# Kernel tuning notes

Measured on AMD Instinct MI355X. Metric: run time of the kernel, lower is better.

Reference implementation:

```python
import jax, jax.numpy as jnp
import numpy as np

DIM = 1024
NUM_HEADS = 16
HEAD_DIM = DIM // NUM_HEADS
SCALE = DIM ** (-0.5)  # NOTE: original scales by full dim, not head_dim


def setup_inputs() -> dict:
    key = jax.random.key(0)
    ks = jax.random.split(key, 5)
    B, S = 2, 2048
    x = jax.random.normal(ks[0], (B, S, DIM), dtype=jnp.float32)
    w_qkv = jax.random.normal(ks[1], (DIM, 3 * DIM), dtype=jnp.float32) * (DIM ** -0.5)
    b_qkv = jax.random.normal(ks[2], (3 * DIM,), dtype=jnp.float32) * 0.02
    w_proj = jax.random.normal(ks[3], (DIM, DIM), dtype=jnp.float32) * (DIM ** -0.5)
    b_proj = jax.random.normal(ks[4], (DIM,), dtype=jnp.float32) * 0.02
    return {"x": x, "w_qkv": w_qkv, "b_qkv": b_qkv, "w_proj": w_proj, "b_proj": b_proj}


def reference(x, w_qkv, b_qkv, w_proj, b_proj):
    B, S, D = x.shape
    qkv = x @ w_qkv + b_qkv                                  # [B,S,3D]
    qkv = qkv.reshape(B, S, NUM_HEADS, 3 * HEAD_DIM).transpose(0, 2, 1, 3)  # [B,H,S,3hd]
    q, k, v = jnp.split(qkv, 3, axis=-1)                     # each [B,H,S,hd]
    attn = jnp.einsum("bhqd,bhkd->bhqk", q, k) * SCALE       # [B,H,S,S]
    attn = jax.nn.softmax(attn, axis=-1)
    out = jnp.einsum("bhqk,bhkd->bhqd", attn, v)             # [B,H,S,hd]
    out = out.transpose(0, 2, 1, 3).reshape(B, S, D)
    return out @ w_proj + b_proj
```

## Files before the change

kernel.cpp:

```cpp
#include <hip/hip_runtime.h>
#include <hip/hip_bf16.h>

#define DIM 1024
#define NH 16
#define HD 64
#define BB 2
#define SS 2048
#define MROWS (BB * SS)
#define SCALE 0.03125f
#define SC_LOG2E 0.04508422002778011f

typedef unsigned short u16;
typedef unsigned int u32;
typedef __attribute__((ext_vector_type(8))) short short8;
typedef __attribute__((ext_vector_type(4))) float f32x4;
typedef __attribute__((ext_vector_type(2))) unsigned int u32x2;

#if __has_builtin(__builtin_amdgcn_exp2f)
#define EXP2(x) __builtin_amdgcn_exp2f(x)
#else
#define EXP2(x) __builtin_exp2f(x)
#endif

__device__ __forceinline__ u16 f2bf(float f) {
  union { float f; u32 u; } v; v.f = f;
  return (u16)((v.u + 0x7fffu + ((v.u >> 16) & 1u)) >> 16);
}

__device__ __forceinline__ u32 pack2bf(float a, float b) {
  union { __hip_bfloat162 h; u32 u; } cv;
  cv.h = __float22bfloat162_rn(make_float2(a, b));
  return cv.u;
}

__device__ __forceinline__ void plswap32(u32& a, u32& b) {
#if __has_builtin(__builtin_amdgcn_permlane32_swap)
  u32x2 t = __builtin_amdgcn_permlane32_swap(a, b, false, false);
  a = t[0]; b = t[1];
#else
  asm("v_permlane32_swap_b32 %0, %1" : "+v"(a), "+v"(b));
#endif
}
__device__ __forceinline__ void plswap16(u32& a, u32& b) {
#if __has_builtin(__builtin_amdgcn_permlane16_swap)
  u32x2 t = __builtin_amdgcn_permlane16_swap(a, b, false, false);
  a = t[0]; b = t[1];
#else
  asm("v_permlane16_swap_b32 %0, %1" : "+v"(a), "+v"(b));
#endif
}

__device__ __forceinline__ void async16(const u16* g, u16* l) {
  __builtin_amdgcn_global_load_lds(
      (const __attribute__((address_space(1))) void*)(const void*)g,
      (__attribute__((address_space(3))) void*)(void*)l, 16, 0, 0);
}

__device__ __forceinline__ short8 ld8(const u16* p) { return *(const short8*)p; }

__global__ void cvt_kernel(const float* __restrict__ in, u16* __restrict__ out, int n4) {
  int i = blockIdx.x * blockDim.x + threadIdx.x;
  if (i < n4) {
    float4 v = ((const float4*)in)[i];
    u32 lo = (u32)f2bf(v.x) | ((u32)f2bf(v.y) << 16);
    u32 hi = (u32)f2bf(v.z) | ((u32)f2bf(v.w) << 16);
    ((uint2*)out)[i] = make_uint2(lo, hi);
  }
}

__global__ void tconv_kernel(const float* __restrict__ in, u16* __restrict__ out, int R, int C) {
  __shared__ u16 t[64 * 65];
  int c0 = blockIdx.x * 64, r0 = blockIdx.y * 64;
  #pragma unroll
  for (int i = 0; i < 16; i++) {
    int j = i * 256 + threadIdx.x;
    int rr = j >> 6, cc = j & 63;
    t[rr * 65 + cc] = f2bf(in[(size_t)(r0 + rr) * C + c0 + cc]);
  }
  __syncthreads();
  #pragma unroll
  for (int i = 0; i < 16; i++) {
    int j = i * 256 + threadIdx.x;
    int oc = j >> 6, orr = j & 63;
    out[(size_t)(c0 + oc) * R + r0 + orr] = t[orr * 65 + oc];
  }
}

template <int MODE>
__global__ __launch_bounds__(256, 2) void gemm_bt(
    const u16* __restrict__ A, const u16* __restrict__ Bt,
    const float* __restrict__ bias, void* __restrict__ C,
    u16* __restrict__ vT, int M, int N, int K) {
  __shared__ __align__(16) u16 As[128 * 32];
  __shared__ __align__(16) u16 Bs[128 * 32];
  const int tid = threadIdx.x;
  const int w = tid >> 6, l = tid & 63;
  const int r = l & 15, q = l >> 4;
  const int m0 = blockIdx.y * 128, n0 = blockIdx.x * 128;
  const int qm = (w & 1) * 64, qn = (w >> 1) * 64;

  const size_t aoff = (size_t)(m0 + w * 16 + (l >> 2)) * K + (size_t)(l & 3) * 8;
  const size_t boff = (size_t)(n0 + w * 16 + (l >> 2)) * K + (size_t)(l & 3) * 8;
  u16* alds = &As[(w * 64 + l) * 8];
  u16* blds = &Bs[(w * 64 + l) * 8];

  f32x4 acc[4][4] = {};
  for (int k0 = 0; k0 < K; k0 += 32) {
    async16(A + aoff + k0, alds);
    async16(A + aoff + (size_t)64 * K + k0, alds + 2048);
    async16(Bt + boff + k0, blds);
    async16(Bt + boff + (size_t)64 * K + k0, blds + 2048);
    __syncthreads();
    short8 af[4], bfr[4];
    #pragma unroll
    for (int i = 0; i < 4; i++) af[i] = ld8(&As[(qm + i * 16 + r) * 32 + q * 8]);
    #pragma unroll
    for (int j = 0; j < 4; j++) bfr[j] = ld8(&Bs[(qn + j * 16 + r) * 32 + q * 8]);
    #pragma unroll
    for (int i = 0; i < 4; i++)
      #pragma unroll
      for (int j = 0; j < 4; j++)
        acc[i][j] = __builtin_amdgcn_mfma_f32_16x16x32_bf16(af[i], bfr[j], acc[i][j], 0, 0, 0);
    __syncthreads();
  }
  #pragma unroll
  for (int i = 0; i < 4; i++) {
    int ro = m0 + qm + i * 16 + q * 4;
    #pragma unroll
    for (int j = 0; j < 4; j++) {
      int col = n0 + qn + j * 16 + r;
      float bv = bias[col];
      float v0 = acc[i][j][0] + bv, v1 = acc[i][j][1] + bv;
      float v2 = acc[i][j][2] + bv, v3 = acc[i][j][3] + bv;
      if (MODE == 1) {
        float* out = (float*)C;
        out[(size_t)(ro + 0) * N + col] = v0;
        out[(size_t)(ro + 1) * N + col] = v1;
        out[(size_t)(ro + 2) * N + col] = v2;
        out[(size_t)(ro + 3) * N + col] = v3;
      } else {
        int h = col / 192, wi = col - h * 192;
        if (wi >= 128) {
          int bb = ro >> 11, s = ro & 2047, d = wi - 128;
          uint2 pk = make_uint2(pack2bf(v0, v1), pack2bf(v2, v3));
          *(uint2*)&vT[((size_t)((bb * NH + h) * HD + d)) * SS + s] = pk;
        } else {
          u16* qk2 = (u16*)C;
          const float sc = (wi < 64) ? SC_LOG2E : 1.0f;
          qk2[(size_t)(ro + 0) * 2048 + h * 128 + wi] = f2bf(v0 * sc);
          qk2[(size_t)(ro + 1) * 2048 + h * 128 + wi] = f2bf(v1 * sc);
          qk2[(size_t)(ro + 2) * 2048 + h * 128 + wi] = f2bf(v2 * sc);
          qk2[(size_t)(ro + 3) * 2048 + h * 128 + wi] = f2bf(v3 * sc);
        }
      }
    }
  }
}

__global__ __launch_bounds__(512, 4) void attn6_kernel(
    const u16* __restrict__ qk2, const u16* __restrict__ vT,
    u16* __restrict__ attno) {
  __shared__ __align__(16) u16 smem[32768];
  const int tid = threadIdx.x;
  const int w = tid >> 6, l = tid & 63;
  const int r = l & 15, q = l >> 4;
  const int wq = w & 3, ws = w >> 2;
  const int lin = blockIdx.x + 16 * (blockIdx.y + 16 * blockIdx.z);
  const int k8 = lin & 7, jj = lin >> 3;
  const int bh = ((jj >> 4) << 3) + k8;
  const int h = bh & 15, b = bh >> 4;
  const int q0 = (jj & 15) * 128;

  const u16* qb = qk2 + (size_t)b * SS * 2048;
  const u16* kB = qb + h * 128 + 64;
  const u16* vB = vT + (size_t)((b * NH + h) * HD) * SS;

  short8 qf[2][2];
  #pragma unroll
  for (int i = 0; i < 2; i++)
    #pragma unroll
    for (int kq = 0; kq < 2; kq++)
      qf[i][kq] = ld8(qb + (size_t)(q0 + wq * 32 + i * 16 + r) * 2048 + h * 128 + kq * 32 + q * 8);

  const int klrow = l >> 3;
  const int kchunk = (l & 7) ^ klrow;
  const int vlrow = l >> 4;
  const int vslot = l & 15;

#define STAGE(KV0, DST) do {                                                     \
    u16* Kd_ = (DST); u16* Vd_ = Kd_ + 8192;                                     \
    _Pragma("unroll")                                                            \
    for (int tt = 0; tt < 2; tt++) {                                             \
      int g = w * 2 + tt;                                                        \
      async16(kB + (size_t)((KV0) + g * 8 + klrow) * 2048 + kchunk * 8,          \
              &Kd_[g * 512 + l * 8]);                                            \
    }                                                                            \
    _Pragma("unroll")                                                            \
    for (int tt = 0; tt < 2; tt++) {                                             \
      int g = w * 2 + tt;                                                        \
      int d_ = g * 4 + vlrow;                                                    \
      int c_ = vslot ^ (d_ & 15);                                                \
      async16(vB + (size_t)d_ * SS + (KV0) + c_ * 8, &Vd_[g * 512 + l * 8]);     \
    }                                                                            \
  } while (0)

#define CONV(ks) do {                                                            \
    _Pragma("unroll")                                                            \
    for (int i = 0; i < 2; i++) {                                                \
      f32x4 sa = sacc[(ks) * 2][i], sb = sacc[(ks) * 2 + 1][i];                  \
      u32 A0 = pack2bf(EXP2(sa[0]), EXP2(sa[1]));                                \
      u32 A1 = pack2bf(EXP2(sa[2]), EXP2(sa[3]));                                \
      u32 B0 = pack2bf(EXP2(sb[0]), EXP2(sb[1]));                                \
      u32 B1 = pack2bf(EXP2(sb[2]), EXP2(sb[3]));                                \
      plswap32(A0, B0);                                                          \
      plswap32(A1, B1);                                                          \
      plswap16(A0, B0);                                                          \
      plswap16(A1, B1);                                                          \
      union { short8 s8; u32 u[4]; } pk;                                         \
      pk.u[0] = A0; pk.u[1] = A1; pk.u[2] = B0; pk.u[3] = B1;                    \
      pa[ks][i] = pk.s8;                                                         \
    }                                                                            \
  } while (0)

#define QKT(j2) do {                                                             \
    const u16* krow = &Ks[(ws * 64 + (j2) * 16 + r) * 64];                       \
    short8 a0 = ld8(krow + ((q ^ (r & 7)) * 8));                                 \
    short8 a1 = ld8(krow + (((4 + q) ^ (r & 7)) * 8));                           \
    __builtin_amdgcn_s_setprio(1);                                               \
    _Pragma("unroll")                                                            \
    for (int i = 0; i < 2; i++) {                                                \
      sacc[j2][i] = __builtin_amdgcn_mfma_f32_16x16x32_bf16(a0, qf[i][0], sacc[j2][i], 0, 0, 0); \
      sacc[j2][i] = __builtin_amdgcn_mfma_f32_16x16x32_bf16(a1, qf[i][1], sacc[j2][i], 0, 0, 0); \
    }                                                                            \
    __builtin_amdgcn_s_setprio(0);                                               \
  } while (0)

#define PV(ks) do {                                                              \
    __builtin_amdgcn_s_setprio(1);                                               \
    den[0] = __builtin_amdgcn_mfma_f32_16x16x32_bf16(pa[ks][0], vone, den[0], 0, 0, 0); \
    den[1] = __builtin_amdgcn_mfma_f32_16x16x32_bf16(pa[ks][1], vone, den[1], 0, 0, 0); \
    _Pragma("unroll")                                                            \
    for (int dj = 0; dj < 4; dj++) {                                             \
      short8 vb = ld8(&Vs[(dj * 16 + r) * 128 + (((ws * 8 + (ks) * 4 + q) ^ r) * 8)]); \
      oacc[0][dj] = __builtin_amdgcn_mfma_f32_16x16x32_bf16(pa[ks][0], vb, oacc[0][dj], 0, 0, 0); \
      oacc[1][dj] = __builtin_amdgcn_mfma_f32_16x16x32_bf16(pa[ks][1], vb, oacc[1][dj], 0, 0, 0); \
    }                                                                            \
    __builtin_amdgcn_s_setprio(0);                                               \
  } while (0)

  const short8 vone = {0x3F80, 0x3F80, 0x3F80, 0x3F80, 0x3F80, 0x3F80, 0x3F80, 0x3F80};
  f32x4 oacc[2][4] = {};
  f32x4 den[2] = {};

  STAGE(0, smem);
  __syncthreads();

  for (int t = 0; t < 16; ++t) {
    const int cur = t & 1;
    u16* Ks = smem + cur * 16384;
    u16* Vs = Ks + 8192;
    if (t < 15) STAGE((t + 1) * 128, smem + (cur ^ 1) * 16384);

    f32x4 sacc[4][2] = {};
    short8 pa[2][2];
    QKT(0); QKT(1);
    CONV(0);
    QKT(2); QKT(3);
    PV(0);
    CONV(1);
    PV(1);
    __syncthreads();
  }
#undef STAGE
#undef CONV
#undef QKT
#undef PV

  float* part = (float*)smem;
  float* dnf  = part + 8 * 32 * 36;
  const int ho = 1 - ws;
  {
    const int wbase = (wq * 2 + ho) * 32;
    #pragma unroll
    for (int i = 0; i < 2; i++) {
      if (ws == 0) {
        *(f32x4*)&part[(wbase + r) * 36 + i * 16 + q * 4]      = oacc[i][2];
        *(f32x4*)&part[(wbase + 16 + r) * 36 + i * 16 + q * 4] = oacc[i][3];
      } else {
        *(f32x4*)&part[(wbase + r) * 36 + i * 16 + q * 4]      = oacc[i][0];
        *(f32x4*)&part[(wbase + 16 + r) * 36 + i * 16 + q * 4] = oacc[i][1];
      }
      if (r == 0)
        *(f32x4*)&dnf[(ws * 4 + wq) * 32 + i * 16 + q * 4] = den[i];
    }
  }
  __syncthreads();
  {
    const int rbase = (wq * 2 + ws) * 32;
    #pragma unroll
    for (int i = 0; i < 2; i++) {
      f32x4 dt = *(f32x4*)&dnf[(ho * 4 + wq) * 32 + i * 16 + q * 4] + den[i];
      f32x4 oa, ob;
      if (ws == 0) { oa = oacc[i][0]; ob = oacc[i][1]; }
      else         { oa = oacc[i][2]; ob = oacc[i][3]; }
      oa += *(f32x4*)&part[(rbase + r) * 36 + i * 16 + q * 4];
      ob += *(f32x4*)&part[(rbase + 16 + r) * 36 + i * 16 + q * 4];
      #pragma unroll
      for (int e = 0; e < 4; e++) {
        float di = 1.f / dt[e];
        int row = q0 + wq * 32 + i * 16 + q * 4 + e;
        u16* o = &attno[(size_t)(b * SS + row) * DIM + h * HD + ws * 32 + r];
        o[0]  = f2bf(oa[e] * di);
        o[16] = f2bf(ob[e] * di);
      }
    }
  }
}

extern "C" void kernel_launch(void* const* d_in, const int* in_sizes, int n_in,
                              void* d_out, int out_size, void* d_ws, size_t ws_size,
                              hipStream_t stream) {
  const float* x      = (const float*)d_in[0];
  const float* w_qkv  = (const float*)d_in[1];
  const float* b_qkv  = (const float*)d_in[2];
  const float* w_proj = (const float*)d_in[3];
  const float* b_proj = (const float*)d_in[4];
  float* out = (float*)d_out;
  char* ws = (char*)d_ws;
  u16* xb     = (u16*)(ws);
  u16* wqkvT  = (u16*)(ws + ((size_t)8  << 20));
  u16* wprojT = (u16*)(ws + ((size_t)14 << 20));
  u16* qk2    = (u16*)(ws + ((size_t)16 << 20));
  u16* attno  = (u16*)(ws + ((size_t)32 << 20));
  u16* vT     = (u16*)(ws + ((size_t)40 << 20));

  cvt_kernel<<<4096, 256, 0, stream>>>(x, xb, MROWS * DIM / 4);
  tconv_kernel<<<dim3(48, 16), 256, 0, stream>>>(w_qkv, wqkvT, DIM, 3 * DIM);
  tconv_kernel<<<dim3(16, 16), 256, 0, stream>>>(w_proj, wprojT, DIM, DIM);
  gemm_bt<0><<<dim3(24, 32), 256, 0, stream>>>(xb, wqkvT, b_qkv, qk2, vT, MROWS, 3 * DIM, DIM);
  attn6_kernel<<<dim3(16, NH, BB), 512, 0, stream>>>(qk2, vT, attno);
  gemm_bt<1><<<dim3(8, 32), 256, 0, stream>>>(attno, wprojT, b_proj, out, nullptr, MROWS, DIM, DIM);
}
```

Before: 189.1 us.

## Double-buffer GEMM LDS stages, add XCD-aware block swizzle and 128x64 projection tiles

The GEMM kernels now double-buffer their shared-memory tiles, so the async global-to-LDS load for the next K step is issued before the MFMAs on the current step. This removes one barrier per iteration. Blocks are launched on a 1D grid and remapped so that consecutive blocks landing on the same XCD (lin & 7) cover adjacent tiles, which should improve L2 reuse. The output projection gets a new 128x64-tile kernel with 512 blocks instead of 256, to fill the 256 CUs better. The cost is double the LDS per block, which can lower occupancy.

```diff
diff --git a/kernel.cpp b/kernel.cpp
--- a/kernel.cpp
+++ b/kernel.cpp
@@ -86,31 +86,41 @@
   }
 }
 
-template <int MODE>
+template <int MODE, int NXB>
 __global__ __launch_bounds__(256, 2) void gemm_bt(
     const u16* __restrict__ A, const u16* __restrict__ Bt,
     const float* __restrict__ bias, void* __restrict__ C,
     u16* __restrict__ vT, int M, int N, int K) {
-  __shared__ __align__(16) u16 As[128 * 32];
-  __shared__ __align__(16) u16 Bs[128 * 32];
+  __shared__ __align__(16) u16 smem[16384];
   const int tid = threadIdx.x;
   const int w = tid >> 6, l = tid & 63;
   const int r = l & 15, q = l >> 4;
-  const int m0 = blockIdx.y * 128, n0 = blockIdx.x * 128;
+  const int nwg = gridDim.x;
+  const int cpx = nwg >> 3;
+  const int lin = blockIdx.x;
+  const int swz = (lin & 7) * cpx + (lin >> 3);
+  const int m0 = (swz / NXB) * 128, n0 = (swz % NXB) * 128;
   const int qm = (w & 1) * 64, qn = (w >> 1) * 64;
 
   const size_t aoff = (size_t)(m0 + w * 16 + (l >> 2)) * K + (size_t)(l & 3) * 8;
   const size_t boff = (size_t)(n0 + w * 16 + (l >> 2)) * K + (size_t)(l & 3) * 8;
-  u16* alds = &As[(w * 64 + l) * 8];
-  u16* blds = &Bs[(w * 64 + l) * 8];
+  const int soff = (w * 64 + l) * 8;
+
+#define GSTAGE(K0, BASE) do {                                                    \
+    u16* As_ = (BASE); u16* Bs_ = As_ + 4096;                                    \
+    async16(A + aoff + (K0), As_ + soff);                                        \
+    async16(A + aoff + (size_t)64 * K + (K0), As_ + soff + 2048);                \
+    async16(Bt + boff + (K0), Bs_ + soff);                                       \
+    async16(Bt + boff + (size_t)64 * K + (K0), Bs_ + soff + 2048);               \
+  } while (0)
 
   f32x4 acc[4][4] = {};
+  GSTAGE(0, smem);
+  __syncthreads();
   for (int k0 = 0; k0 < K; k0 += 32) {
-    async16(A + aoff + k0, alds);
-    async16(A + aoff + (size_t)64 * K + k0, alds + 2048);
-    async16(Bt + boff + k0, blds);
-    async16(Bt + boff + (size_t)64 * K + k0, blds + 2048);
-    __syncthreads();
+    u16* As = smem + ((k0 >> 5) & 1) * 8192;
+    u16* Bs = As + 4096;
+    if (k0 + 32 < K) GSTAGE(k0 + 32, smem + ((((k0 >> 5) & 1) ^ 1) * 8192));
     short8 af[4], bfr[4];
     #pragma unroll
     for (int i = 0; i < 4; i++) af[i] = ld8(&As[(qm + i * 16 + r) * 32 + q * 8]);
@@ -123,6 +133,7 @@
         acc[i][j] = __builtin_amdgcn_mfma_f32_16x16x32_bf16(af[i], bfr[j], acc[i][j], 0, 0, 0);
     __syncthreads();
   }
+#undef GSTAGE
   #pragma unroll
   for (int i = 0; i < 4; i++) {
     int ro = m0 + qm + i * 16 + q * 4;
@@ -157,6 +168,68 @@
   }
 }
 
+__global__ __launch_bounds__(256, 4) void gemm_bt_n64(
+    const u16* __restrict__ A, const u16* __restrict__ Bt,
+    const float* __restrict__ bias, float* __restrict__ C,
+    int M, int N, int K) {
+  __shared__ __align__(16) u16 smem[12288];
+  const int tid = threadIdx.x;
+  const int w = tid >> 6, l = tid & 63;
+  const int r = l & 15, q = l >> 4;
+  const int NXB = N >> 6;
+  const int nwg = gridDim.x;
+  const int cpx = nwg >> 3;
+  const int lin = blockIdx.x;
+  const int swz = (lin & 7) * cpx + (lin >> 3);
+  const int m0 = (swz / NXB) * 128, n0 = (swz % NXB) * 64;
+  const int qm = (w & 1) * 64, qn = (w >> 1) * 32;
+
+  const size_t aoff = (size_t)(m0 + w * 16 + (l >> 2)) * K + (size_t)(l & 3) * 8;
+  const size_t boff = (size_t)(n0 + w * 16 + (l >> 2)) * K + (size_t)(l & 3) * 8;
+  const int soff = (w * 64 + l) * 8;
+
+#define NSTAGE(K0, BASE) do {                                                    \
+    u16* As_ = (BASE); u16* Bs_ = As_ + 4096;                                    \
+    async16(A + aoff + (K0), As_ + soff);                                        \
+    async16(A + aoff + (size_t)64 * K + (K0), As_ + soff + 2048);                \
+    async16(Bt + boff + (K0), Bs_ + soff);                                       \
+  } while (0)
+
+  f32x4 acc[4][2] = {};
+  NSTAGE(0, smem);
+  __syncthreads();
+  for (int k0 = 0; k0 < K; k0 += 32) {
+    u16* As = smem + ((k0 >> 5) & 1) * 6144;
+    u16* Bs = As + 4096;
+    if (k0 + 32 < K) NSTAGE(k0 + 32, smem + ((((k0 >> 5) & 1) ^ 1) * 6144));
+    short8 af[4], bfr[2];
+    #pragma unroll
+    for (int i = 0; i < 4; i++) af[i] = ld8(&As[(qm + i * 16 + r) * 32 + q * 8]);
+    #pragma unroll
+    for (int j = 0; j < 2; j++) bfr[j] = ld8(&Bs[(qn + j * 16 + r) * 32 + q * 8]);
+    #pragma unroll
+    for (int i = 0; i < 4; i++)
+      #pragma unroll
+      for (int j = 0; j < 2; j++)
+        acc[i][j] = __builtin_amdgcn_mfma_f32_16x16x32_bf16(af[i], bfr[j], acc[i][j], 0, 0, 0);
+    __syncthreads();
+  }
+#undef NSTAGE
+  #pragma unroll
+  for (int i = 0; i < 4; i++) {
+    int ro = m0 + qm + i * 16 + q * 4;
+    #pragma unroll
+    for (int j = 0; j < 2; j++) {
+      int col = n0 + qn + j * 16 + r;
+      float bv = bias[col];
+      C[(size_t)(ro + 0) * N + col] = acc[i][j][0] + bv;
+      C[(size_t)(ro + 1) * N + col] = acc[i][j][1] + bv;
+      C[(size_t)(ro + 2) * N + col] = acc[i][j][2] + bv;
+      C[(size_t)(ro + 3) * N + col] = acc[i][j][3] + bv;
+    }
+  }
+}
+
 __global__ __launch_bounds__(512, 4) void attn6_kernel(
     const u16* __restrict__ qk2, const u16* __restrict__ vT,
     u16* __restrict__ attno) {
@@ -337,7 +410,7 @@
   cvt_kernel<<<4096, 256, 0, stream>>>(x, xb, MROWS * DIM / 4);
   tconv_kernel<<<dim3(48, 16), 256, 0, stream>>>(w_qkv, wqkvT, DIM, 3 * DIM);
   tconv_kernel<<<dim3(16, 16), 256, 0, stream>>>(w_proj, wprojT, DIM, DIM);
-  gemm_bt<0><<<dim3(24, 32), 256, 0, stream>>>(xb, wqkvT, b_qkv, qk2, vT, MROWS, 3 * DIM, DIM);
+  gemm_bt<0, 24><<<768, 256, 0, stream>>>(xb, wqkvT, b_qkv, qk2, vT, MROWS, 3 * DIM, DIM);
   attn6_kernel<<<dim3(16, NH, BB), 512, 0, stream>>>(qk2, vT, attno);
-  gemm_bt<1><<<dim3(8, 32), 256, 0, stream>>>(attno, wprojT, b_proj, out, nullptr, MROWS, DIM, DIM);
-}
+  gemm_bt_n64<<<512, 256, 0, stream>>>(attno, wprojT, b_proj, out, MROWS, DIM, DIM);
+}
```

New measurement: 181.9 us. 1.04x faster.

## Rework GEMMs with 128x64 tiles, LDS double-buffering, swizzle and block remapping

Applied to the files above, without the earlier changes.

Replaces the 128x128 GEMM with a 128x64-tile variant that double-buffers LDS, issuing the next k-slice's async loads before computing the current one, so there is one barrier per iteration. It XOR-swizzles the LDS chunk layout to reduce bank conflicts, remaps the 1D grid so neighbouring blocks land on the same XCD, and raises the occupancy hint to 4 blocks per CU. The smaller tile doubles the block count for better CU fill but lowers arithmetic intensity per block.

```diff
diff --git a/kernel.cpp b/kernel.cpp
--- a/kernel.cpp
+++ b/kernel.cpp
@@ -86,48 +86,62 @@
   }
 }
 
-template <int MODE>
-__global__ __launch_bounds__(256, 2) void gemm_bt(
+template <int MODE, int NXB>
+__global__ __launch_bounds__(256, 4) void gemm_n64(
     const u16* __restrict__ A, const u16* __restrict__ Bt,
     const float* __restrict__ bias, void* __restrict__ C,
     u16* __restrict__ vT, int M, int N, int K) {
-  __shared__ __align__(16) u16 As[128 * 32];
-  __shared__ __align__(16) u16 Bs[128 * 32];
+  __shared__ __align__(16) u16 smem[12288];
   const int tid = threadIdx.x;
   const int w = tid >> 6, l = tid & 63;
   const int r = l & 15, q = l >> 4;
-  const int m0 = blockIdx.y * 128, n0 = blockIdx.x * 128;
-  const int qm = (w & 1) * 64, qn = (w >> 1) * 64;
-
-  const size_t aoff = (size_t)(m0 + w * 16 + (l >> 2)) * K + (size_t)(l & 3) * 8;
-  const size_t boff = (size_t)(n0 + w * 16 + (l >> 2)) * K + (size_t)(l & 3) * 8;
-  u16* alds = &As[(w * 64 + l) * 8];
-  u16* blds = &Bs[(w * 64 + l) * 8];
-
-  f32x4 acc[4][4] = {};
+  const int nwg = gridDim.x;
+  const int cpx = nwg >> 3;
+  const int lin = blockIdx.x;
+  const int swz = (lin & 7) * cpx + (lin >> 3);
+  const int m0 = (swz / NXB) * 128, n0 = (swz % NXB) * 64;
+  const int qm = (w & 1) * 64, qn = (w >> 1) * 32;
+
+  const int gchunk = (l & 3) ^ ((l >> 3) & 3);
+  const size_t aoff = (size_t)(m0 + w * 16 + (l >> 2)) * K + (size_t)gchunk * 8;
+  const size_t boff = (size_t)(n0 + w * 16 + (l >> 2)) * K + (size_t)gchunk * 8;
+  const int soff = (w * 64 + l) * 8;
+  const int xq = (r >> 1) & 3;
+
+#define NSTAGE(K0, BASE) do {                                                    \
+    u16* As_ = (BASE); u16* Bs_ = As_ + 4096;                                    \
+    async16(A + aoff + (K0), As_ + soff);                                        \
+    async16(A + aoff + (size_t)64 * K + (K0), As_ + soff + 2048);                \
+    async16(Bt + boff + (K0), Bs_ + soff);                                       \
+  } while (0)
+
+  f32x4 acc[4][2] = {};
+  NSTAGE(0, smem);
+  __syncthreads();
   for (int k0 = 0; k0 < K; k0 += 32) {
-    async16(A + aoff + k0, alds);
-    async16(A + aoff + (size_t)64 * K + k0, alds + 2048);
-    async16(Bt + boff + k0, blds);
-    async16(Bt + boff + (size_t)64 * K + k0, blds + 2048);
-    __syncthreads();
-    short8 af[4], bfr[4];
-    #pragma unroll
-    for (int i = 0; i < 4; i++) af[i] = ld8(&As[(qm + i * 16 + r) * 32 + q * 8]);
-    #pragma unroll
-    for (int j = 0; j < 4; j++) bfr[j] = ld8(&Bs[(qn + j * 16 + r) * 32 + q * 8]);
+    u16* As = smem + ((k0 >> 5) & 1) * 6144;
+    u16* Bs = As + 4096;
+    if (k0 + 32 < K) NSTAGE(k0 + 32, smem + ((((k0 >> 5) & 1) ^ 1) * 6144));
+    short8 af[4], bfr[2];
+    #pragma unroll
+    for (int i = 0; i < 4; i++)
+      af[i] = ld8(&As[(qm + i * 16 + r) * 32 + (q ^ xq) * 8]);
+    #pragma unroll
+    for (int j = 0; j < 2; j++)
+      bfr[j] = ld8(&Bs[(qn + j * 16 + r) * 32 + (q ^ xq) * 8]);
     #pragma unroll
     for (int i = 0; i < 4; i++)
       #pragma unroll
-      for (int j = 0; j < 4; j++)
+      for (int j = 0; j < 2; j++)
         acc[i][j] = __builtin_amdgcn_mfma_f32_16x16x32_bf16(af[i], bfr[j], acc[i][j], 0, 0, 0);
     __syncthreads();
   }
+#undef NSTAGE
   #pragma unroll
   for (int i = 0; i < 4; i++) {
     int ro = m0 + qm + i * 16 + q * 4;
     #pragma unroll
-    for (int j = 0; j < 4; j++) {
+    for (int j = 0; j < 2; j++) {
       int col = n0 + qn + j * 16 + r;
       float bv = bias[col];
       float v0 = acc[i][j][0] + bv, v1 = acc[i][j][1] + bv;
@@ -337,7 +351,7 @@
   cvt_kernel<<<4096, 256, 0, stream>>>(x, xb, MROWS * DIM / 4);
   tconv_kernel<<<dim3(48, 16), 256, 0, stream>>>(w_qkv, wqkvT, DIM, 3 * DIM);
   tconv_kernel<<<dim3(16, 16), 256, 0, stream>>>(w_proj, wprojT, DIM, DIM);
-  gemm_bt<0><<<dim3(24, 32), 256, 0, stream>>>(xb, wqkvT, b_qkv, qk2, vT, MROWS, 3 * DIM, DIM);
+  gemm_n64<0, 48><<<1536, 256, 0, stream>>>(xb, wqkvT, b_qkv, qk2, vT, MROWS, 3 * DIM, DIM);
   attn6_kernel<<<dim3(16, NH, BB), 512, 0, stream>>>(qk2, vT, attno);
-  gemm_bt<1><<<dim3(8, 32), 256, 0, stream>>>(attno, wprojT, b_proj, out, nullptr, MROWS, DIM, DIM);
-}
+  gemm_n64<1, 16><<<512, 256, 0, stream>>>(attno, wprojT, b_proj, out, nullptr, MROWS, DIM, DIM);
+}
```

Result: no change. 192.5 us (+1.8%).

## Double-buffer GEMM with BK=64, XOR-swizzled LDS, XCD-aware block remap

Applied to the files above, without the earlier changes.

Rewrites both GEMMs to use a K-tile of 64 with double-buffered LDS, so the next tile's async loads are issued before computing on the current one, which removes one barrier per step. LDS columns are XOR-swizzled to avoid bank conflicts, and block indices are remapped across the eight XCDs for cache locality. The projection GEMM switches to 128x64 tiles to launch more workgroups. LDS use grows, which could limit occupancy.

```diff
diff --git a/kernel.cpp b/kernel.cpp
--- a/kernel.cpp
+++ b/kernel.cpp
@@ -86,48 +86,72 @@
   }
 }
 
-template <int MODE>
-__global__ __launch_bounds__(256, 2) void gemm_bt(
+template <int MODE, int BN, int NXB>
+__global__ __launch_bounds__(256, (BN == 128 ? 2 : 3)) void gemm_bk64(
     const u16* __restrict__ A, const u16* __restrict__ Bt,
     const float* __restrict__ bias, void* __restrict__ C,
     u16* __restrict__ vT, int M, int N, int K) {
-  __shared__ __align__(16) u16 As[128 * 32];
-  __shared__ __align__(16) u16 Bs[128 * 32];
+  constexpr int JN = BN / 32;
+  constexpr int BTI = BN / 32;
+  constexpr int BUF = 8192 + BN * 64;
+  __shared__ __align__(16) u16 smem[2 * BUF];
   const int tid = threadIdx.x;
   const int w = tid >> 6, l = tid & 63;
   const int r = l & 15, q = l >> 4;
-  const int m0 = blockIdx.y * 128, n0 = blockIdx.x * 128;
-  const int qm = (w & 1) * 64, qn = (w >> 1) * 64;
-
-  const size_t aoff = (size_t)(m0 + w * 16 + (l >> 2)) * K + (size_t)(l & 3) * 8;
-  const size_t boff = (size_t)(n0 + w * 16 + (l >> 2)) * K + (size_t)(l & 3) * 8;
-  u16* alds = &As[(w * 64 + l) * 8];
-  u16* blds = &Bs[(w * 64 + l) * 8];
-
-  f32x4 acc[4][4] = {};
-  for (int k0 = 0; k0 < K; k0 += 32) {
-    async16(A + aoff + k0, alds);
-    async16(A + aoff + (size_t)64 * K + k0, alds + 2048);
-    async16(Bt + boff + k0, blds);
-    async16(Bt + boff + (size_t)64 * K + k0, blds + 2048);
+  const int nwg = gridDim.x;
+  const int cpx = nwg >> 3;
+  const int lin = blockIdx.x;
+  const int swz = (lin & 7) * cpx + (lin >> 3);
+  const int m0 = (swz / NXB) * 128, n0 = (swz % NXB) * BN;
+  const int qm = (w & 1) * 64, qn = (w >> 1) * (BN / 2);
+
+  const int gc = (l & 7) ^ (l >> 3);
+  const size_t aoffb = (size_t)(m0 + w * 32 + (l >> 3)) * K + (size_t)gc * 8;
+  const size_t boffb = (size_t)(n0 + w * (BN / 4) + (l >> 3)) * K + (size_t)gc * 8;
+  const int xs = r & 7;
+
+#define GSTAGE(K0, BASE) do {                                                    \
+    u16* As_ = (BASE); u16* Bs_ = As_ + 8192;                                    \
+    _Pragma("unroll")                                                            \
+    for (int t = 0; t < 4; t++)                                                  \
+      async16(A + aoffb + (size_t)t * 8 * K + (K0), As_ + w * 2048 + t * 512 + l * 8); \
+    _Pragma("unroll")                                                            \
+    for (int t = 0; t < BTI; t++)                                                \
+      async16(Bt + boffb + (size_t)t * 8 * K + (K0), Bs_ + w * (BN * 16) + t * 512 + l * 8); \
+  } while (0)
+
+  f32x4 acc[4][JN] = {};
+  GSTAGE(0, smem);
+  __syncthreads();
+  for (int k0 = 0; k0 < K; k0 += 64) {
+    u16* As = smem + ((k0 >> 6) & 1) * BUF;
+    u16* Bs = As + 8192;
+    if (k0 + 64 < K) GSTAGE(k0 + 64, smem + ((((k0 >> 6) & 1) ^ 1) * BUF));
+    short8 af[2][4], bfr[2][JN];
+    #pragma unroll
+    for (int kq = 0; kq < 2; kq++) {
+      #pragma unroll
+      for (int i = 0; i < 4; i++)
+        af[kq][i] = ld8(&As[(qm + i * 16 + r) * 64 + (((kq * 4 + q) ^ xs) * 8)]);
+      #pragma unroll
+      for (int j = 0; j < JN; j++)
+        bfr[kq][j] = ld8(&Bs[(qn + j * 16 + r) * 64 + (((kq * 4 + q) ^ xs) * 8)]);
+    }
+    #pragma unroll
+    for (int kq = 0; kq < 2; kq++)
+      #pragma unroll
+      for (int i = 0; i < 4; i++)
+        #pragma unroll
+        for (int j = 0; j < JN; j++)
+          acc[i][j] = __builtin_amdgcn_mfma_f32_16x16x32_bf16(af[kq][i], bfr[kq][j], acc[i][j], 0, 0, 0);
     __syncthreads();
-    short8 af[4], bfr[4];
-    #pragma unroll
-    for (int i = 0; i < 4; i++) af[i] = ld8(&As[(qm + i * 16 + r) * 32 + q * 8]);
-    #pragma unroll
-    for (int j = 0; j < 4; j++) bfr[j] = ld8(&Bs[(qn + j * 16 + r) * 32 + q * 8]);
-    #pragma unroll
-    for (int i = 0; i < 4; i++)
-      #pragma unroll
-      for (int j = 0; j < 4; j++)
-        acc[i][j] = __builtin_amdgcn_mfma_f32_16x16x32_bf16(af[i], bfr[j], acc[i][j], 0, 0, 0);
-    __syncthreads();
-  }
+  }
+#undef GSTAGE
   #pragma unroll
   for (int i = 0; i < 4; i++) {
     int ro = m0 + qm + i * 16 + q * 4;
     #pragma unroll
-    for (int j = 0; j < 4; j++) {
+    for (int j = 0; j < JN; j++) {
       int col = n0 + qn + j * 16 + r;
       float bv = bias[col];
       float v0 = acc[i][j][0] + bv, v1 = acc[i][j][1] + bv;
@@ -337,7 +361,7 @@
   cvt_kernel<<<4096, 256, 0, stream>>>(x, xb, MROWS * DIM / 4);
   tconv_kernel<<<dim3(48, 16), 256, 0, stream>>>(w_qkv, wqkvT, DIM, 3 * DIM);
   tconv_kernel<<<dim3(16, 16), 256, 0, stream>>>(w_proj, wprojT, DIM, DIM);
-  gemm_bt<0><<<dim3(24, 32), 256, 0, stream>>>(xb, wqkvT, b_qkv, qk2, vT, MROWS, 3 * DIM, DIM);
+  gemm_bk64<0, 128, 24><<<768, 256, 0, stream>>>(xb, wqkvT, b_qkv, qk2, vT, MROWS, 3 * DIM, DIM);
   attn6_kernel<<<dim3(16, NH, BB), 512, 0, stream>>>(qk2, vT, attno);
-  gemm_bt<1><<<dim3(8, 32), 256, 0, stream>>>(attno, wprojT, b_proj, out, nullptr, MROWS, DIM, DIM);
-}
+  gemm_bk64<1, 64, 16><<<512, 256, 0, stream>>>(attno, wprojT, b_proj, out, nullptr, MROWS, DIM, DIM);
+}
```

Result: faster. 177.0 us (-6.4%).
